# Kernel tuning notes

Measured on AMD Instinct MI355X. Metric: run time of the kernel, lower is better.

Reference implementation:

```python
import jax, jax.numpy as jnp
import numpy as np

P = 5  # patchsize == stride (non-overlapping)


def unfold_patches(x, p):
    # x: [N, C, H, W] -> [N, L, C, p, p], blocks ordered row-major (matches F.unfold)
    N, C, H, W = x.shape
    x = x.reshape(N, C, H // p, p, W // p, p)
    return x.transpose(0, 2, 4, 1, 3, 5).reshape(N, (H // p) * (W // p), C, p, p)


def fold_patches(pat, H, W, p):
    # [N, L, C, p, p] -> [N, C, H, W]; stride==kernel so F.fold is pure placement (no overlap sums)
    N, L, C, _, _ = pat.shape
    x = pat.reshape(N, H // p, W // p, C, p, p)
    return x.transpose(0, 3, 1, 4, 2, 5).reshape(N, C, H, W)


def gather_scale_concat(fold, idx, gamma):
    # fold: [N, L, C, p, p]; idx: [N, L, 4] int; gamma: [4]
    def gath(k):
        return jnp.take_along_axis(fold, idx[:, :, k][:, :, None, None, None], axis=1)
    # first slot uses patch j itself (not idx[...,0]), per the original loop body
    return jnp.concatenate(
        [gamma[0] * fold, gamma[1] * gath(1), gamma[2] * gath(2), gamma[3] * gath(3)], axis=2)


def conv3x3(x, w, b):
    y = jax.lax.conv_general_dilated(x, w, window_strides=(1, 1), padding='SAME',
                                     dimension_numbers=('NCHW', 'OIHW', 'NCHW'))
    return y + b[None, :, None, None]


def setup_inputs() -> dict:
    key = jax.random.key(0)
    ks = jax.random.split(key, 7)
    N, C, H, W = 4, 32, 300, 300
    L = (H // P) * (W // P)
    x_rgb = jax.random.normal(ks[0], (N, C, H, W), dtype=jnp.float32)
    y_hsi = jax.random.normal(ks[1], (N, C, H, W), dtype=jnp.float32)
    corr = jax.random.randint(ks[2], (2, N, L, 4), 0, L)
    rgb_gamma = jnp.ones((4,), jnp.float32)
    hsi_gamma = jnp.ones((4,), jnp.float32)
    rgb_W = jax.random.normal(ks[3], (C, 4 * C, 3, 3), dtype=jnp.float32) * 0.02
    rgb_b = jnp.zeros((C,), jnp.float32)
    hsi_W = jax.random.normal(ks[4], (C, 4 * C, 3, 3), dtype=jnp.float32) * 0.02
    hsi_b = jnp.zeros((C,), jnp.float32)
    return {'x_rgb': x_rgb, 'y_hsi': y_hsi, 'corr': corr,
            'rgb_gamma': rgb_gamma, 'hsi_gamma': hsi_gamma,
            'rgb_W': rgb_W, 'rgb_b': rgb_b, 'hsi_W': hsi_W, 'hsi_b': hsi_b}


def reference(x_rgb, y_hsi, corr, rgb_gamma, hsi_gamma, rgb_W, rgb_b, hsi_W, hsi_b):
    n_feats = x_rgb.shape[1]
    half = n_feats // 2
    H, W = x_rgb.shape[2], x_rgb.shape[3]
    hsi = jnp.concatenate([x_rgb[:, :half], y_hsi[:, :half]], axis=1)      # [N, n_feats, H, W]
    rgb = jnp.concatenate([x_rgb[:, half:n_feats], y_hsi[:, half:n_feats]], axis=1)
    idx = corr[0]  # [N, L, 4]
    # H, W divisible by P -> calc_padding yields zero padding
    fold_rgb = unfold_patches(rgb, P)  # [N, L, C, p, p]
    fold_hsi = unfold_patches(hsi, P)
    patch_rgb = gather_scale_concat(fold_rgb, idx, rgb_gamma)  # [N, L, 4C, p, p]
    patch_hsi = gather_scale_concat(fold_hsi, idx, hsi_gamma)
    img_rgb = fold_patches(patch_rgb, H, W, P)  # [N, 4C, H, W]
    img_hsi = fold_patches(patch_hsi, H, W, P)
    out_rgb = conv3x3(img_rgb, rgb_W, rgb_b) + rgb
    out_hsi = conv3x3(img_hsi, hsi_W, hsi_b) + hsi
    return (out_rgb, out_hsi)
```

## Files before the change

### kernel.cpp

```cpp
#include <hip/hip_runtime.h>

#define HW        90000
#define OUT_HALF  11520000
#define CPLANE    11520000ull
#define WPACK_OFF  46080000ull
#define WS_NEED    (46080000ull + 147456ull)

typedef short short8 __attribute__((ext_vector_type(8)));
typedef float f32x4  __attribute__((ext_vector_type(4)));

__device__ inline short f2bf(float f) {
    unsigned u = __builtin_bit_cast(unsigned, f);
    u += 0x7fff + ((u >> 16) & 1);
    return (short)(u >> 16);
}
__device__ inline float bf2f(short s) {
    unsigned u = ((unsigned)(unsigned short)s) << 16;
    return __builtin_bit_cast(float, u);
}

__global__ __launch_bounds__(256)
void pack_weights(const float* __restrict__ wR, const float* __restrict__ wH,
                  const float* __restrict__ rg, const float* __restrict__ hg,
                  short* __restrict__ wpack) {
    int id = blockIdx.x * 256 + threadIdx.x;
    if (id >= 73728) return;
    int e    = id & 7;
    int lane = (id >> 3) & 63;
    int h    = (id >> 9) & 1;
    int t    = (id >> 10) % 9;
    int kb   = ((id >> 10) / 9) & 3;
    int conv = id / 36864;
    int co   = h * 16 + (lane & 15);
    int cin  = kb * 32 + (lane >> 4) * 8 + e;
    const float* w = conv ? wH : wR;
    const float* g = conv ? hg : rg;
    wpack[id] = f2bf(w[(co * 128 + cin) * 9 + t] * g[cin >> 5]);
}

__global__ __launch_bounds__(256)
void nchw2nhwc(const float* __restrict__ xrgb, const float* __restrict__ yhsi,
               short* __restrict__ cmb) {
    int wave = threadIdx.x >> 6, lane = threadIdx.x & 63;
    if (lane >= 60) return;
    int y = blockIdx.y * 4 + wave;
    int x = blockIdx.x * 60 + lane;
    int n = blockIdx.z;
    const float* xb = xrgb + n * 32 * HW + y * 300 + x;
    const float* yb = yhsi + n * 32 * HW + y * 300 + x;
    size_t pxo = ((size_t)n * HW + y * 300 + x) * 32;
    short* d0 = cmb + pxo;
    short* d1 = cmb + CPLANE + pxo;
    #pragma unroll
    for (int q = 0; q < 4; ++q) {
        short8 v0, v1;
        #pragma unroll
        for (int e = 0; e < 8; ++e) {
            int c = q * 8 + e;
            v0[e] = f2bf((c < 16) ? xb[(16 + c) * HW] : yb[c * HW]);
            v1[e] = f2bf((c < 16) ? xb[c * HW] : yb[(c - 16) * HW]);
        }
        *(short8*)(d0 + q * 8) = v0;
        *(short8*)(d1 + q * 8) = v1;
    }
}

__global__ __launch_bounds__(256, 3)
void conv_mfma(const short* __restrict__ cmb_all, const short* __restrict__ wpack,
               const int* __restrict__ corr,
               const float* __restrict__ bR, const float* __restrict__ bH,
               float* __restrict__ out) {
    __shared__ alignas(16) char lds[2][20736];
    int tile = blockIdx.x;
    int n = blockIdx.y;
    int conv = blockIdx.z;
    int ty = tile / 19, tx = tile - ty * 19;
    int y0 = ty * 16, x0 = tx * 16;
    int tid = threadIdx.x;

    const short* cmb = cmb_all + conv * CPLANE + (size_t)n * HW * 32;
    const short* wp  = wpack + conv * 36864;

    int  pA = tid, pB = tid + 256;
    bool hasB = pB < 324;
    bool vA = false, vB = false;
    int sA0=0,sA1=0,sA2=0,sA3=0, sB0=0,sB1=0,sB2=0,sB3=0;
    {
        int hr = pA / 18, hc = pA - hr * 18;
        int gy = y0 + hr - 1, gx = x0 + hc - 1;
        vA = (gy >= 0 && gy < 300 && gx >= 0 && gx < 300);
        if (vA) {
            int pr = gy / 5, pc = gx / 5;
            int sj = pr * 60 + pc;
            int sintra = (gy - pr * 5) * 300 + (gx - pc * 5);
            const int* scr = corr + (n * 3600 + sj) * 4;
            int j1 = scr[1], j2 = scr[2], j3 = scr[3];
            sA0 = (sj / 60) * 1500 + (sj % 60) * 5 + sintra;
            sA1 = (j1 / 60) * 1500 + (j1 % 60) * 5 + sintra;
            sA2 = (j2 / 60) * 1500 + (j2 % 60) * 5 + sintra;
            sA3 = (j3 / 60) * 1500 + (j3 % 60) * 5 + sintra;
        }
    }
    if (hasB) {
        int hr = pB / 18, hc = pB - hr * 18;
        int gy = y0 + hr - 1, gx = x0 + hc - 1;
        vB = (gy >= 0 && gy < 300 && gx >= 0 && gx < 300);
        if (vB) {
            int pr = gy / 5, pc = gx / 5;
            int sj = pr * 60 + pc;
            int sintra = (gy - pr * 5) * 300 + (gx - pc * 5);
            const int* scr = corr + (n * 3600 + sj) * 4;
            int j1 = scr[1], j2 = scr[2], j3 = scr[3];
            sB0 = (sj / 60) * 1500 + (sj % 60) * 5 + sintra;
            sB1 = (j1 / 60) * 1500 + (j1 % 60) * 5 + sintra;
            sB2 = (j2 / 60) * 1500 + (j2 % 60) * 5 + sintra;
            sB3 = (j3 / 60) * 1500 + (j3 % 60) * 5 + sintra;
        }
    }

    #define STAGE1(buf, px, valid, soff)                                         \
        do {                                                                     \
            short8 v0 = {0,0,0,0,0,0,0,0}, v1 = v0, v2 = v0, v3 = v0;            \
            if (valid) {                                                         \
                const short8* s = (const short8*)(cmb + (size_t)(soff) * 32);    \
                v0 = s[0]; v1 = s[1]; v2 = s[2]; v3 = s[3];                      \
            }                                                                    \
            char* d = lds[(buf)];                                                \
            int b0 = (px) * 64, sz = ((px) & 7) << 4;                            \
            *(short8*)(d + ((b0 +  0) ^ sz)) = v0;                               \
            *(short8*)(d + ((b0 + 16) ^ sz)) = v1;                               \
            *(short8*)(d + ((b0 + 32) ^ sz)) = v2;                               \
            *(short8*)(d + ((b0 + 48) ^ sz)) = v3;                               \
        } while (0)
    #define STAGE(buf, k)                                                        \
        do {                                                                     \
            STAGE1(buf, pA, vA, sA##k);                                          \
            if (hasB) STAGE1(buf, pB, vB, sB##k);                                \
        } while (0)

    STAGE(0, 0);
    __syncthreads();

    int wave = tid >> 6, lane = tid & 63;
    int l15 = lane & 15, lh = lane >> 4;
    int wr = wave * 4;

    f32x4 acc[4][2];
    #pragma unroll
    for (int g = 0; g < 4; ++g)
        #pragma unroll
        for (int h = 0; h < 2; ++h)
            acc[g][h] = (f32x4){0.f, 0.f, 0.f, 0.f};

    #pragma unroll
    for (int kb = 0; kb < 4; ++kb) {
        if (kb == 0) STAGE(1, 1);
        if (kb == 1) STAGE(0, 2);
        if (kb == 2) STAGE(1, 3);
        const char* base = lds[kb & 1];
        #pragma unroll
        for (int dxi = 0; dxi < 3; ++dxi) {
            short8 a[3][2];
            #pragma unroll
            for (int dyi = 0; dyi < 3; ++dyi) {
                int t = dyi * 3 + dxi;
                a[dyi][0] = *(const short8*)(wp + (((kb * 9 + t) * 2 + 0) * 64 + lane) * 8);
                a[dyi][1] = *(const short8*)(wp + (((kb * 9 + t) * 2 + 1) * 64 + lane) * 8);
            }
            short8 b[6];
            #pragma unroll
            for (int rr = 0; rr < 6; ++rr) {
                int hp = (wr + rr) * 18 + (l15 + dxi);
                b[rr] = *(const short8*)(base + ((hp * 64 + lh * 16) ^ ((hp & 7) << 4)));
            }
            #pragma unroll
            for (int g = 0; g < 4; ++g) {
                #pragma unroll
                for (int dyi = 0; dyi < 3; ++dyi) {
                    acc[g][0] = __builtin_amdgcn_mfma_f32_16x16x32_bf16(a[dyi][0], b[g + dyi], acc[g][0], 0, 0, 0);
                    acc[g][1] = __builtin_amdgcn_mfma_f32_16x16x32_bf16(a[dyi][1], b[g + dyi], acc[g][1], 0, 0, 0);
                }
            }
        }
        if (kb < 3) __syncthreads();
    }

    const float* bias = conv ? bH : bR;
    #pragma unroll
    for (int g = 0; g < 4; ++g) {
        int gy = y0 + wr + g;
        int gx = x0 + l15;
        if (gy < 300 && gx < 300) {
            int pixo = gy * 300 + gx;
            const short* resp = cmb + (size_t)pixo * 32;
            short8 r0 = *(const short8*)(resp);
            short8 r1 = *(const short8*)(resp + 8);
            short8 r2 = *(const short8*)(resp + 16);
            short8 r3 = *(const short8*)(resp + 24);
            #pragma unroll
            for (int h = 0; h < 2; ++h) {
                #pragma unroll
                for (int reg = 0; reg < 4; ++reg) {
                    int co = h * 16 + lh * 4 + reg;
                    int q = co >> 3, e = co & 7;
                    float res = bf2f(q == 0 ? r0[e] : q == 1 ? r1[e] : q == 2 ? r2[e] : r3[e]);
                    out[conv * OUT_HALF + (n * 32 + co) * HW + pixo] = acc[g][h][reg] + bias[co] + res;
                }
            }
        }
    }
    #undef STAGE
    #undef STAGE1
}

__global__ __launch_bounds__(256)
void fused_gather_conv(const float* __restrict__ xrgb, const float* __restrict__ yhsi,
                       const int* __restrict__ corr, const float* __restrict__ rgb_gamma,
                       const float* __restrict__ hsi_gamma, const float* __restrict__ wR,
                       const float* __restrict__ bR, const float* __restrict__ wH,
                       const float* __restrict__ bH, float* __restrict__ out) {
    int tid = blockIdx.x * blockDim.x + threadIdx.x;
    if (tid >= 4 * HW) return;
    int n = tid / HW, pix = tid - n * HW;
    int y = pix / 300, x = pix - y * 300;
    const int* idx = corr + n * (3600 * 4);
    const float* xb = xrgb + n * (32 * HW);
    const float* yb = yhsi + n * (32 * HW);
    float accR[32], accH[32];
    #pragma unroll
    for (int i = 0; i < 32; ++i) { accR[i] = 0.f; accH[i] = 0.f; }
    for (int k = 0; k < 4; ++k) {
        float gr = rgb_gamma[k], gh = hsi_gamma[k];
        int off[9];
        #pragma unroll
        for (int t = 0; t < 9; ++t) {
            int dy = t / 3 - 1, dx = t % 3 - 1;
            int yy = y + dy, xx = x + dx;
            int o = -1;
            if (yy >= 0 && yy < 300 && xx >= 0 && xx < 300) {
                int pr = yy / 5, pc = xx / 5;
                int j = pr * 60 + pc;
                int jp = (k == 0) ? j : idx[j * 4 + k];
                o = ((jp / 60) * 5 + (yy - pr * 5)) * 300 + (jp % 60) * 5 + (xx - pc * 5);
            }
            off[t] = o;
        }
        for (int c = 0; c < 32; ++c) {
            const float* srcR = (c < 16) ? (xb + (16 + c) * HW) : (yb + c * HW);
            const float* srcH = (c < 16) ? (xb + c * HW) : (yb + (c - 16) * HW);
            float vr[9], vh[9];
            #pragma unroll
            for (int t = 0; t < 9; ++t) {
                bool vld = off[t] >= 0;
                vr[t] = vld ? gr * srcR[off[t]] : 0.f;
                vh[t] = vld ? gh * srcH[off[t]] : 0.f;
            }
            const float* wRp = wR + (k * 32 + c) * 9;
            const float* wHp = wH + (k * 32 + c) * 9;
            #pragma unroll
            for (int t = 0; t < 9; ++t)
                #pragma unroll
                for (int co = 0; co < 32; ++co) {
                    accR[co] = fmaf(vr[t], wRp[co * 1152 + t], accR[co]);
                    accH[co] = fmaf(vh[t], wHp[co * 1152 + t], accH[co]);
                }
        }
    }
    #pragma unroll
    for (int co = 0; co < 32; ++co) {
        float resR = (co < 16) ? xb[(16 + co) * HW + pix] : yb[co * HW + pix];
        float resH = (co < 16) ? xb[co * HW + pix] : yb[(co - 16) * HW + pix];
        out[(n * 32 + co) * HW + pix]            = accR[co] + bR[co] + resR;
        out[OUT_HALF + (n * 32 + co) * HW + pix] = accH[co] + bH[co] + resH;
    }
}

extern "C" void kernel_launch(void* const* d_in, const int* in_sizes, int n_in,
                              void* d_out, int out_size, void* d_ws, size_t ws_size,
                              hipStream_t stream) {
    const float* xrgb = (const float*)d_in[0];
    const float* yhsi = (const float*)d_in[1];
    const int*   corr = (const int*)d_in[2];
    const float* rg   = (const float*)d_in[3];
    const float* hg   = (const float*)d_in[4];
    const float* wR   = (const float*)d_in[5];
    const float* bR   = (const float*)d_in[6];
    const float* wH   = (const float*)d_in[7];
    const float* bH   = (const float*)d_in[8];
    float* out = (float*)d_out;

    if (ws_size >= WS_NEED) {
        short* cmb   = (short*)d_ws;
        short* wpack = (short*)((char*)d_ws + WPACK_OFF);
        hipLaunchKernelGGL(pack_weights, dim3(288), dim3(256), 0, stream, wR, wH, rg, hg, wpack);
        hipLaunchKernelGGL(nchw2nhwc, dim3(5, 75, 4), dim3(256), 0, stream, xrgb, yhsi, cmb);
        hipLaunchKernelGGL(conv_mfma, dim3(361, 4, 2), dim3(256), 0, stream,
                           cmb, wpack, corr, bR, bH, out);
    } else {
        int total = 4 * HW;
        hipLaunchKernelGGL(fused_gather_conv, dim3((total + 255) / 256), dim3(256), 0, stream,
                           xrgb, yhsi, corr, rg, hg, wR, bR, wH, bH, out);
    }
}
```

Before: 137.8 us.

## Stage gathered conv input tiles via direct global-to-LDS loads

Replaces register-staged gathers (global load into VGPRs, then swizzled LDS store) with the global_load_lds builtin, which writes 16-byte chunks straight into shared memory. Each wave issues up to six 1KB chunk loads per stage, with lane-to-pixel/chunk mapping precomputed to reproduce the XOR swizzle. Out-of-bounds pixels read from a zeroed 64-byte workspace buffer set by an extra memset. This aims to cut VGPR pressure and LDS write instructions and to let loads overlap MFMA work. The cost is a slightly larger LDS buffer and more per-thread address state.

```diff
diff --git a/kernel.cpp b/kernel.cpp
--- a/kernel.cpp
+++ b/kernel.cpp
@@ -4,10 +4,12 @@
 #define OUT_HALF  11520000
 #define CPLANE    11520000ull
 #define WPACK_OFF  46080000ull
-#define WS_NEED    (46080000ull + 147456ull)
+#define ZOFF       46227456ull
+#define WS_NEED    (46227456ull + 64ull)
 
 typedef short short8 __attribute__((ext_vector_type(8)));
 typedef float f32x4  __attribute__((ext_vector_type(4)));
+typedef unsigned int u32;
 
 __device__ inline short f2bf(float f) {
     unsigned u = __builtin_bit_cast(unsigned, f);
@@ -17,6 +19,11 @@
 __device__ inline float bf2f(short s) {
     unsigned u = ((unsigned)(unsigned short)s) << 16;
     return __builtin_bit_cast(float, u);
+}
+__device__ inline void gload16(char* ldst, const short* gsrc) {
+    __builtin_amdgcn_global_load_lds(
+        (const __attribute__((address_space(1))) u32*)gsrc,
+        (__attribute__((address_space(3))) u32*)ldst, 16, 0, 0);
 }
 
 __global__ __launch_bounds__(256)
@@ -67,81 +74,72 @@
 
 __global__ __launch_bounds__(256, 3)
 void conv_mfma(const short* __restrict__ cmb_all, const short* __restrict__ wpack,
-               const int* __restrict__ corr,
+               const int* __restrict__ corr, const short* __restrict__ zbuf,
                const float* __restrict__ bR, const float* __restrict__ bH,
                float* __restrict__ out) {
-    __shared__ alignas(16) char lds[2][20736];
+    __shared__ alignas(16) char lds[2][21504];
     int tile = blockIdx.x;
     int n = blockIdx.y;
     int conv = blockIdx.z;
     int ty = tile / 19, tx = tile - ty * 19;
     int y0 = ty * 16, x0 = tx * 16;
     int tid = threadIdx.x;
+    int wave = tid >> 6, lane = tid & 63;
 
     const short* cmb = cmb_all + conv * CPLANE + (size_t)n * HW * 32;
     const short* wp  = wpack + conv * 36864;
 
-    int  pA = tid, pB = tid + 256;
-    bool hasB = pB < 324;
-    bool vA = false, vB = false;
-    int sA0=0,sA1=0,sA2=0,sA3=0, sB0=0,sB1=0,sB2=0,sB3=0;
-    {
-        int hr = pA / 18, hc = pA - hr * 18;
-        int gy = y0 + hr - 1, gx = x0 + hc - 1;
-        vA = (gy >= 0 && gy < 300 && gx >= 0 && gx < 300);
-        if (vA) {
-            int pr = gy / 5, pc = gx / 5;
-            int sj = pr * 60 + pc;
-            int sintra = (gy - pr * 5) * 300 + (gx - pc * 5);
-            const int* scr = corr + (n * 3600 + sj) * 4;
-            int j1 = scr[1], j2 = scr[2], j3 = scr[3];
-            sA0 = (sj / 60) * 1500 + (sj % 60) * 5 + sintra;
-            sA1 = (j1 / 60) * 1500 + (j1 % 60) * 5 + sintra;
-            sA2 = (j2 / 60) * 1500 + (j2 % 60) * 5 + sintra;
-            sA3 = (j3 / 60) * 1500 + (j3 % 60) * 5 + sintra;
-        }
-    }
-    if (hasB) {
-        int hr = pB / 18, hc = pB - hr * 18;
-        int gy = y0 + hr - 1, gx = x0 + hc - 1;
-        vB = (gy >= 0 && gy < 300 && gx >= 0 && gx < 300);
-        if (vB) {
-            int pr = gy / 5, pc = gx / 5;
-            int sj = pr * 60 + pc;
-            int sintra = (gy - pr * 5) * 300 + (gx - pc * 5);
-            const int* scr = corr + (n * 3600 + sj) * 4;
-            int j1 = scr[1], j2 = scr[2], j3 = scr[3];
-            sB0 = (sj / 60) * 1500 + (sj % 60) * 5 + sintra;
-            sB1 = (j1 / 60) * 1500 + (j1 % 60) * 5 + sintra;
-            sB2 = (j2 / 60) * 1500 + (j2 % 60) * 5 + sintra;
-            sB3 = (j3 / 60) * 1500 + (j3 % 60) * 5 + sintra;
-        }
-    }
-
-    #define STAGE1(buf, px, valid, soff)                                         \
-        do {                                                                     \
-            short8 v0 = {0,0,0,0,0,0,0,0}, v1 = v0, v2 = v0, v3 = v0;            \
-            if (valid) {                                                         \
-                const short8* s = (const short8*)(cmb + (size_t)(soff) * 32);    \
-                v0 = s[0]; v1 = s[1]; v2 = s[2]; v3 = s[3];                      \
-            }                                                                    \
-            char* d = lds[(buf)];                                                \
-            int b0 = (px) * 64, sz = ((px) & 7) << 4;                            \
-            *(short8*)(d + ((b0 +  0) ^ sz)) = v0;                               \
-            *(short8*)(d + ((b0 + 16) ^ sz)) = v1;                               \
-            *(short8*)(d + ((b0 + 32) ^ sz)) = v2;                               \
-            *(short8*)(d + ((b0 + 48) ^ sz)) = v3;                               \
-        } while (0)
+    int  psoff[6][4];
+    int  gaddr_c[6];
+    bool pvalid[6];
+    #pragma unroll
+    for (int ji = 0; ji < 6; ++ji) {
+        pvalid[ji] = false;
+        gaddr_c[ji] = 0;
+        psoff[ji][0] = psoff[ji][1] = psoff[ji][2] = psoff[ji][3] = 0;
+        int j = wave + ji * 4;
+        if (j < 21) {
+            int off = j * 1024 + lane * 16;
+            int pxp = off >> 6;
+            int pxl = pxp ^ ((pxp >> 2) & 1);
+            int cl  = ((off >> 4) & 3) ^ (pxl & 3);
+            gaddr_c[ji] = cl * 8;
+            if (pxl < 324) {
+                int hr = pxl / 18, hc = pxl - hr * 18;
+                int gy = y0 + hr - 1, gx = x0 + hc - 1;
+                if (gy >= 0 && gy < 300 && gx >= 0 && gx < 300) {
+                    pvalid[ji] = true;
+                    int pr = gy / 5, pc = gx / 5;
+                    int sj = pr * 60 + pc;
+                    int sintra = (gy - pr * 5) * 300 + (gx - pc * 5);
+                    const int* scr = corr + (n * 3600 + sj) * 4;
+                    int j1 = scr[1], j2 = scr[2], j3 = scr[3];
+                    psoff[ji][0] = (sj / 60) * 1500 + (sj % 60) * 5 + sintra;
+                    psoff[ji][1] = (j1 / 60) * 1500 + (j1 % 60) * 5 + sintra;
+                    psoff[ji][2] = (j2 / 60) * 1500 + (j2 % 60) * 5 + sintra;
+                    psoff[ji][3] = (j3 / 60) * 1500 + (j3 % 60) * 5 + sintra;
+                }
+            }
+        }
+    }
+
     #define STAGE(buf, k)                                                        \
         do {                                                                     \
-            STAGE1(buf, pA, vA, sA##k);                                          \
-            if (hasB) STAGE1(buf, pB, vB, sB##k);                                \
+            _Pragma("unroll")                                                    \
+            for (int ji = 0; ji < 6; ++ji) {                                     \
+                int j = wave + ji * 4;                                           \
+                if (j < 21) {                                                    \
+                    const short* g = pvalid[ji]                                  \
+                        ? (cmb + (size_t)psoff[ji][k] * 32 + gaddr_c[ji])        \
+                        : (zbuf + gaddr_c[ji]);                                  \
+                    gload16(&lds[buf][j * 1024], g);                             \
+                }                                                                \
+            }                                                                    \
         } while (0)
 
     STAGE(0, 0);
     __syncthreads();
 
-    int wave = tid >> 6, lane = tid & 63;
     int l15 = lane & 15, lh = lane >> 4;
     int wr = wave * 4;
 
@@ -210,7 +208,6 @@
         }
     }
     #undef STAGE
-    #undef STAGE1
 }
 
 __global__ __launch_bounds__(256)
@@ -292,10 +289,12 @@
     if (ws_size >= WS_NEED) {
         short* cmb   = (short*)d_ws;
         short* wpack = (short*)((char*)d_ws + WPACK_OFF);
+        short* zbuf  = (short*)((char*)d_ws + ZOFF);
+        hipMemsetAsync((char*)d_ws + ZOFF, 0, 64, stream);
         hipLaunchKernelGGL(pack_weights, dim3(288), dim3(256), 0, stream, wR, wH, rg, hg, wpack);
         hipLaunchKernelGGL(nchw2nhwc, dim3(5, 75, 4), dim3(256), 0, stream, xrgb, yhsi, cmb);
         hipLaunchKernelGGL(conv_mfma, dim3(361, 4, 2), dim3(256), 0, stream,
-                           cmb, wpack, corr, bR, bH, out);
+                           cmb, wpack, corr, zbuf, bR, bH, out);
     } else {
         int total = 4 * HW;
         hipLaunchKernelGGL(fused_gather_conv, dim3((total + 255) / 256), dim3(256), 0, stream,
```

New measurement: 138.4 us. Within noise of the previous version (+0.4%).
